# Optimization experiments

Measured on AMD Instinct MI355X. Metric: run time of the kernel, lower is better.

The kernel has to match this reference:

```python
import jax, jax.numpy as jnp
import numpy as np

N, L, D, H, MLP_MULT = 2, 384, 512, 8, 4
HD = D // H
DM = D * MLP_MULT
EPS = 1e-5


def _linear_params(key, out_dim, in_dim, scale=0.02):
    kw, kb = jax.random.split(key)
    w = jax.random.normal(kw, (out_dim, in_dim), jnp.float32) * scale
    b = jax.random.normal(kb, (out_dim,), jnp.float32) * scale
    return w, b


def setup_inputs() -> dict:
    key = jax.random.key(0)
    ks = jax.random.split(key, 12)
    x = jax.random.normal(ks[0], (N, L, D), jnp.float32)
    mem = jax.random.normal(ks[1], (N, L, D), jnp.float32)
    pairwise_distances = jax.random.normal(ks[2], (N, L, L, D), jnp.float32)
    mem_padding_mask = jax.random.randint(ks[3], (N, L), 0, 2).astype(bool)
    qw, qb = _linear_params(ks[4], D, D)
    kvw, kvb = _linear_params(ks[5], 2 * D, D)
    pw, pb = _linear_params(ks[6], D, D)
    edw, edb = _linear_params(ks[7], H, D)
    w1, b1 = _linear_params(ks[8], DM, D)
    w2, b2 = _linear_params(ks[9], DM, DM)
    w3, b3 = _linear_params(ks[10], D, DM)
    return {
        'x': x, 'mem': mem, 'pairwise_distances': pairwise_distances,
        'mem_padding_mask': mem_padding_mask,
        'qw': qw, 'qb': qb, 'kvw': kvw, 'kvb': kvb, 'pw': pw, 'pb': pb,
        'edw': edw, 'edb': edb,
        'ln1_g': jnp.ones((D,), jnp.float32), 'ln1_b': jnp.zeros((D,), jnp.float32),
        'ln2_g': jnp.ones((D,), jnp.float32), 'ln2_b': jnp.zeros((D,), jnp.float32),
        'w1': w1, 'b1': b1, 'w2': w2, 'b2': b2, 'w3': w3, 'b3': b3,
    }


def _layernorm(x, g, b):
    m = jnp.mean(x, axis=-1, keepdims=True)
    v = jnp.mean((x - m) ** 2, axis=-1, keepdims=True)
    return (x - m) * jax.lax.rsqrt(v + EPS) * g + b


def reference(x, mem, pairwise_distances, mem_padding_mask,
              qw, qb, kvw, kvb, pw, pb, edw, edb,
              ln1_g, ln1_b, ln2_g, ln2_b,
              w1, b1, w2, b2, w3, b3):
    scale = HD ** -0.5
    a_in = _layernorm(x, ln1_g, ln1_b)
    a_mem = _layernorm(mem, ln1_g, ln1_b)

    q = (a_in @ qw.T + qb).reshape(N, L, H, HD).transpose(0, 2, 1, 3)   # (N,H,L1,HD)
    kv = (a_mem @ kvw.T + kvb).reshape(N, L, 2, H, HD)
    k = kv[:, :, 0].transpose(0, 2, 1, 3)                               # (N,H,L2,HD)
    v = kv[:, :, 1].transpose(0, 2, 1, 3)

    scores = jnp.einsum('bhid,bhjd->bhij', q, k) * scale                # (N,H,L1,L2)

    # T5-style relative position bias from pairwise distances
    bias = (pairwise_distances @ edw.T + edb)                            # (N,L1,L2,H)
    scores = scores + bias.transpose(0, 3, 1, 2)

    # padding mask (True = padded); rows that are fully padded get a zero
    # mask instead (then their output is zeroed after attention)
    all_pad = jnp.all(mem_padding_mask, axis=-1)                         # (N,)
    neg_inf = jnp.asarray(-jnp.inf, scores.dtype)
    mask = jnp.where(mem_padding_mask[:, None, None, :], neg_inf, 0.0)
    mask = jnp.where(all_pad[:, None, None, None], 0.0, mask)
    scores = scores + mask

    attn = jax.nn.softmax(scores, axis=-1)
    out = jnp.einsum('bhij,bhjd->bhid', attn, v)                         # (N,H,L1,HD)
    out = out * (~all_pad)[:, None, None, None]
    out = out.transpose(0, 2, 1, 3).reshape(N, L, D)

    x = x + (out @ pw.T + pb)

    h = _layernorm(x, ln2_g, ln2_b)
    h = jax.nn.silu(h @ w1.T + b1)
    h = jax.nn.silu(h @ w2.T + b2)
    h = h @ w3.T + b3
    return x + h
```

## Files before the change

### kernel.cpp

```cpp
#include <hip/hip_runtime.h>
#include <hip/hip_bf16.h>
#include <math.h>

#define NB   2
#define LSEQ 384
#define DMODEL 512
#define NH   8
#define HD2  64
#define DMLP 2048
#define LL2  (LSEQ*LSEQ)
#define ROWS (NB*LSEQ)

using bf16x8 = __attribute__((ext_vector_type(8))) short;
using f32x4  = __attribute__((ext_vector_type(4))) float;

__device__ __forceinline__ unsigned short f2bf(float f) {
    union { __hip_bfloat16 h; unsigned short u; } cv;
    cv.h = __float2bfloat16(f);
    return cv.u;
}

__device__ __forceinline__ void gload_lds16(const void* g, void* l) {
    __builtin_amdgcn_global_load_lds(
        (const __attribute__((address_space(1))) void*)g,
        (__attribute__((address_space(3))) void*)l, 16, 0, 0);
}

__global__ __launch_bounds__(256) void pre_kernel(
        const float* __restrict__ x, const float* __restrict__ mem,
        const float* __restrict__ ln1g, const float* __restrict__ ln1b,
        unsigned short* __restrict__ a_in, unsigned short* __restrict__ a_mem,
        const float* __restrict__ s0, const float* __restrict__ s1,
        const float* __restrict__ s2, const float* __restrict__ s3,
        const float* __restrict__ s4, const float* __restrict__ s5,
        const float* __restrict__ edw,
        unsigned short* __restrict__ d0, unsigned short* __restrict__ d1,
        unsigned short* __restrict__ d2, unsigned short* __restrict__ d3,
        unsigned short* __restrict__ d4, unsigned short* __restrict__ d5,
        unsigned short* __restrict__ edwb) {
    const int tid = threadIdx.x;
    if (blockIdx.x < 384) {
        int lane = tid & 63;
        int row  = blockIdx.x * 4 + (tid >> 6);
        const float* src = (row < ROWS) ? x : mem;
        unsigned short* dst = (row < ROWS) ? a_in : a_mem;
        int r2 = (row < ROWS) ? row : row - ROWS;
        const float* p = src + (size_t)r2 * DMODEL + lane * 8;
        float4 v0 = *(const float4*)p;
        float4 v1 = *(const float4*)(p + 4);
        float s  = v0.x + v0.y + v0.z + v0.w + v1.x + v1.y + v1.z + v1.w;
        float ss = v0.x*v0.x + v0.y*v0.y + v0.z*v0.z + v0.w*v0.w
                 + v1.x*v1.x + v1.y*v1.y + v1.z*v1.z + v1.w*v1.w;
        #pragma unroll
        for (int o = 32; o; o >>= 1) { s += __shfl_xor(s, o); ss += __shfl_xor(ss, o); }
        float m   = s * (1.0f / DMODEL);
        float var = ss * (1.0f / DMODEL) - m * m;
        float r   = rsqrtf(var + 1e-5f);
        float4 g0 = *(const float4*)(ln1g + lane * 8);
        float4 g1 = *(const float4*)(ln1g + lane * 8 + 4);
        float4 b0 = *(const float4*)(ln1b + lane * 8);
        float4 b1 = *(const float4*)(ln1b + lane * 8 + 4);
        unsigned short* q = dst + (size_t)r2 * DMODEL + lane * 8;
        ushort4 lo = {f2bf((v0.x-m)*r*g0.x+b0.x), f2bf((v0.y-m)*r*g0.y+b0.y),
                      f2bf((v0.z-m)*r*g0.z+b0.z), f2bf((v0.w-m)*r*g0.w+b0.w)};
        ushort4 hi = {f2bf((v1.x-m)*r*g1.x+b1.x), f2bf((v1.y-m)*r*g1.y+b1.y),
                      f2bf((v1.z-m)*r*g1.z+b1.z), f2bf((v1.w-m)*r*g1.w+b1.w)};
        *(ushort4*)q = lo;
        *(ushort4*)(q + 4) = hi;
        return;
    }
    const int stride = (gridDim.x - 384) * 256;
    const int t0 = (blockIdx.x - 384) * 256 + tid;
    const float* srcs[6] = {s0, s1, s2, s3, s4, s5};
    unsigned short* dsts[6] = {d0, d1, d2, d3, d4, d5};
    const int nf4[6] = {DMODEL*DMODEL/4, 2*DMODEL*DMODEL/4, DMODEL*DMODEL/4,
                        DMLP*DMODEL/4, DMLP*DMLP/4, DMLP*DMODEL/4};
    #pragma unroll
    for (int a = 0; a < 6; a++) {
        const float* s = srcs[a];
        unsigned short* d = dsts[a];
        for (int i = t0; i < nf4[a]; i += stride) {
            float4 v = *(const float4*)(s + (size_t)i * 4);
            ushort4 o = {f2bf(v.x), f2bf(v.y), f2bf(v.z), f2bf(v.w)};
            *(ushort4*)(d + (size_t)i * 4) = o;
        }
    }
    for (int i = t0; i < 16 * 512 / 4; i += stride) {
        int row = i >> 7;
        float4 v = {0.f, 0.f, 0.f, 0.f};
        if (row < 8) v = *(const float4*)(edw + (size_t)i * 4);
        ushort4 o = {f2bf(v.x), f2bf(v.y), f2bf(v.z), f2bf(v.w)};
        *(ushort4*)(edwb + (size_t)i * 4) = o;
    }
}

__global__ __launch_bounds__(256) void ln_kernel(const float* __restrict__ src0,
                                                 const float* __restrict__ g,
                                                 const float* __restrict__ b,
                                                 unsigned short* __restrict__ dst0) {
    int lane = threadIdx.x & 63;
    int row  = blockIdx.x * 4 + (threadIdx.x >> 6);
    const float* p = src0 + (size_t)row * DMODEL + lane * 8;
    float4 v0 = *(const float4*)p;
    float4 v1 = *(const float4*)(p + 4);
    float s  = v0.x + v0.y + v0.z + v0.w + v1.x + v1.y + v1.z + v1.w;
    float ss = v0.x*v0.x + v0.y*v0.y + v0.z*v0.z + v0.w*v0.w
             + v1.x*v1.x + v1.y*v1.y + v1.z*v1.z + v1.w*v1.w;
    #pragma unroll
    for (int o = 32; o; o >>= 1) { s += __shfl_xor(s, o); ss += __shfl_xor(ss, o); }
    float m   = s * (1.0f / DMODEL);
    float var = ss * (1.0f / DMODEL) - m * m;
    float r   = rsqrtf(var + 1e-5f);
    float4 g0 = *(const float4*)(g + lane * 8);
    float4 g1 = *(const float4*)(g + lane * 8 + 4);
    float4 b0 = *(const float4*)(b + lane * 8);
    float4 b1 = *(const float4*)(b + lane * 8 + 4);
    unsigned short* q = dst0 + (size_t)row * DMODEL + lane * 8;
    ushort4 lo = {f2bf((v0.x-m)*r*g0.x+b0.x), f2bf((v0.y-m)*r*g0.y+b0.y),
                  f2bf((v0.z-m)*r*g0.z+b0.z), f2bf((v0.w-m)*r*g0.w+b0.w)};
    ushort4 hi = {f2bf((v1.x-m)*r*g1.x+b1.x), f2bf((v1.y-m)*r*g1.y+b1.y),
                  f2bf((v1.z-m)*r*g1.z+b1.z), f2bf((v1.w-m)*r*g1.w+b1.w)};
    *(ushort4*)q = lo;
    *(ushort4*)(q + 4) = hi;
}

__global__ __launch_bounds__(256) void bias_mfma(const float* __restrict__ pd,
                                                 const unsigned short* __restrict__ edwb,
                                                 const float* __restrict__ edb,
                                                 const int* __restrict__ mask,
                                                 float* __restrict__ biasb) {
    __shared__ float Asb[3][64 * 64];
    const int tid = threadIdx.x;
    const int lane = tid & 63, w = tid >> 6;
    const int T = blockIdx.x;
    const size_t row0 = (size_t)T * 64;
    const int n = T / 2304;
    const int rem64 = (T - n * 2304) * 64;
    const int i = rem64 / LSEQ, j0 = rem64 % LSEQ;

    const int c = lane & 15, g = lane >> 4;
    bf16x8 bfv[8][2];
    #pragma unroll
    for (int kc = 0; kc < 8; kc++)
        #pragma unroll
        for (int ks = 0; ks < 2; ks++)
            bfv[kc][ks] = *(const bf16x8*)&edwb[c * 512 + kc * 64 + ks * 32 + g * 8];

    int pad = 1;
    for (int j = lane; j < LSEQ; j += 64) pad &= (mask[n * LSEQ + j] != 0) ? 1 : 0;
    unsigned long long bal = __ballot(pad);
    const int ap = (bal == ~0ull) ? 1 : 0;

    int rr[4], sc[4];
    #pragma unroll
    for (int q = 0; q < 4; q++) {
        int s = q * 256 + tid;
        rr[q] = s >> 4;
        int cs = s & 15;
        sc[q] = (cs & 8) | ((cs & 7) ^ (rr[q] & 7));
    }

    f32x4 acc = {};

    #pragma unroll
    for (int q = 0; q < 4; q++)
        gload_lds16(pd + (row0 + rr[q]) * DMODEL + sc[q] * 4, &Asb[0][(q * 256 + tid) * 4]);
    #pragma unroll
    for (int q = 0; q < 4; q++)
        gload_lds16(pd + (row0 + rr[q]) * DMODEL + 64 + sc[q] * 4, &Asb[1][(q * 256 + tid) * 4]);

    #pragma unroll
    for (int kc = 0; kc < 8; kc++) {
        if (kc < 7) asm volatile("s_waitcnt vmcnt(4)" ::: "memory");
        else        asm volatile("s_waitcnt vmcnt(0)" ::: "memory");
        __builtin_amdgcn_s_barrier();
        __builtin_amdgcn_sched_barrier(0);
        if (kc + 2 < 8) {
            const int nb = (kc + 2) % 3;
            #pragma unroll
            for (int q = 0; q < 4; q++)
                gload_lds16(pd + (row0 + rr[q]) * DMODEL + (kc + 2) * 64 + sc[q] * 4,
                            &Asb[nb][(q * 256 + tid) * 4]);
        }
        const float* Ab = &Asb[kc % 3][0];
        #pragma unroll
        for (int ks = 0; ks < 2; ks++) {
            const int ch0 = (8 * ks) | ((2 * g) ^ (c & 7));
            const int ch1 = (8 * ks) | ((2 * g + 1) ^ (c & 7));
            float4 a0 = *(const float4*)&Ab[(w * 16 + c) * 64 + ch0 * 4];
            float4 a1 = *(const float4*)&Ab[(w * 16 + c) * 64 + ch1 * 4];
            bf16x8 af;
            af[0] = (short)f2bf(a0.x); af[1] = (short)f2bf(a0.y);
            af[2] = (short)f2bf(a0.z); af[3] = (short)f2bf(a0.w);
            af[4] = (short)f2bf(a1.x); af[5] = (short)f2bf(a1.y);
            af[6] = (short)f2bf(a1.z); af[7] = (short)f2bf(a1.w);
            acc = __builtin_amdgcn_mfma_f32_16x16x32_bf16(af, bfv[kc][ks], acc, 0, 0, 0);
        }
    }

    if (c < 8) {
        const float eb = edb[c];
        const int jj = j0 + w * 16 + g * 4;
        int4 mv = *(const int4*)&mask[n * LSEQ + jj];
        const float NEGINF = -__builtin_inff();
        float4 o;
        o.x = acc[0] + eb + ((!ap && mv.x) ? NEGINF : 0.0f);
        o.y = acc[1] + eb + ((!ap && mv.y) ? NEGINF : 0.0f);
        o.z = acc[2] + eb + ((!ap && mv.z) ? NEGINF : 0.0f);
        o.w = acc[3] + eb + ((!ap && mv.w) ? NEGINF : 0.0f);
        *(float4*)&biasb[(size_t)(n * 8 + c) * LL2 + (size_t)i * LSEQ + jj] = o;
    }
}

template<int ACT, int RES, int OBF>
__device__ __forceinline__ void gemm_body(const unsigned short* __restrict__ A,
        const unsigned short* __restrict__ W, const float* __restrict__ bv,
        const float* __restrict__ Rsd, void* __restrict__ Cv,
        int Nn, int K, int m0, int n0, short* As, short* Ws) {
    const int tid  = threadIdx.x;
    const int lane = tid & 63, w = tid >> 6;
    const int wr = w >> 1, wc = w & 1;
    const int s0 = tid, s1 = 256 + tid;
    const int r0 = s0 >> 3, c0 = ((s0 & 7) ^ (r0 & 7)) << 3;
    const int r1 = s1 >> 3, c1 = ((s1 & 7) ^ (r1 & 7)) << 3;
    const unsigned short* ag0 = A + (size_t)(m0 + r0) * K + c0;
    const unsigned short* ag1 = A + (size_t)(m0 + r1) * K + c1;
    const unsigned short* wg0 = W + (size_t)(n0 + r0) * K + c0;
    const unsigned short* wg1 = W + (size_t)(n0 + r1) * K + c1;

    f32x4 acc[2][2] = {};
    const int lc = lane & 15, lr = lane >> 4;
    const int KT = K >> 6;

    #pragma unroll
    for (int t = 0; t < 4; t++) {
        const int b = t * 4096, k0 = t << 6;
        gload_lds16(ag0 + k0, &As[b + s0 * 8]);
        gload_lds16(ag1 + k0, &As[b + s1 * 8]);
        gload_lds16(wg0 + k0, &Ws[b + s0 * 8]);
        gload_lds16(wg1 + k0, &Ws[b + s1 * 8]);
    }

    for (int t = 0; t < KT; t++) {
        int rem = KT - 1 - t; if (rem > 3) rem = 3;
        if (rem >= 3)      asm volatile("s_waitcnt vmcnt(12)" ::: "memory");
        else if (rem == 2) asm volatile("s_waitcnt vmcnt(8)"  ::: "memory");
        else if (rem == 1) asm volatile("s_waitcnt vmcnt(4)"  ::: "memory");
        else               asm volatile("s_waitcnt vmcnt(0)"  ::: "memory");
        __builtin_amdgcn_s_barrier();
        __builtin_amdgcn_sched_barrier(0);
        const int cur = (t & 3) * 4096;
        bf16x8 af[2][2], bfr[2][2];
        #pragma unroll
        for (int m = 0; m < 2; m++) {
            const int rra = wr * 32 + m * 16 + lc;
            #pragma unroll
            for (int kk = 0; kk < 2; kk++) {
                const int cc = (lr + kk * 4) ^ (rra & 7);
                af[m][kk] = *(const bf16x8*)&As[cur + rra * 64 + cc * 8];
            }
        }
        #pragma unroll
        for (int nn = 0; nn < 2; nn++) {
            const int rrb = wc * 32 + nn * 16 + lc;
            #pragma unroll
            for (int kk = 0; kk < 2; kk++) {
                const int cc = (lr + kk * 4) ^ (rrb & 7);
                bfr[nn][kk] = *(const bf16x8*)&Ws[cur + rrb * 64 + cc * 8];
            }
        }
        #pragma unroll
        for (int m = 0; m < 2; m++)
            #pragma unroll
            for (int nn = 0; nn < 2; nn++) {
                acc[m][nn] = __builtin_amdgcn_mfma_f32_16x16x32_bf16(af[m][0], bfr[nn][0], acc[m][nn], 0, 0, 0);
                acc[m][nn] = __builtin_amdgcn_mfma_f32_16x16x32_bf16(af[m][1], bfr[nn][1], acc[m][nn], 0, 0, 0);
            }
        if (t + 4 < KT) {
            __builtin_amdgcn_sched_barrier(0);
            __builtin_amdgcn_s_barrier();
            const int b = cur, k0 = (t + 4) << 6;
            gload_lds16(ag0 + k0, &As[b + s0 * 8]);
            gload_lds16(ag1 + k0, &As[b + s1 * 8]);
            gload_lds16(wg0 + k0, &Ws[b + s0 * 8]);
            gload_lds16(wg1 + k0, &Ws[b + s1 * 8]);
        }
    }

    #pragma unroll
    for (int nn = 0; nn < 2; nn++) {
        int gcol = n0 + wc * 32 + nn * 16 + lc;
        float bb = bv[gcol];
        #pragma unroll
        for (int m = 0; m < 2; m++) {
            #pragma unroll
            for (int r = 0; r < 4; r++) {
                int grow = m0 + wr * 32 + m * 16 + lr * 4 + r;
                float o = acc[m][nn][r] + bb;
                if (ACT) o = o / (1.0f + expf(-o));
                if (RES) o += Rsd[(size_t)grow * Nn + gcol];
                if (OBF) ((unsigned short*)Cv)[(size_t)grow * Nn + gcol] = f2bf(o);
                else     ((float*)Cv)[(size_t)grow * Nn + gcol] = o;
            }
        }
    }
}

template<int ACT, int RES, int OBF>
__global__ __launch_bounds__(256) void mfma_gemm(const unsigned short* __restrict__ A,
                                                 const unsigned short* __restrict__ W,
                                                 const float* __restrict__ bv,
                                                 const float* __restrict__ Rsd,
                                                 void* __restrict__ Cv, int Nn, int K) {
    __shared__ short As[4 * 4096];
    __shared__ short Ws[4 * 4096];
    gemm_body<ACT, RES, OBF>(A, W, bv, Rsd, Cv, Nn, K, blockIdx.y * 64, blockIdx.x * 64, As, Ws);
}

__global__ __launch_bounds__(256) void qkv_gemm(const unsigned short* __restrict__ a_in,
                                                const unsigned short* __restrict__ a_mem,
                                                const unsigned short* __restrict__ qwb,
                                                const unsigned short* __restrict__ kvwb,
                                                const float* __restrict__ qbv,
                                                const float* __restrict__ kvbv,
                                                float* __restrict__ qbuf,
                                                float* __restrict__ kvbuf) {
    __shared__ short As[4 * 4096];
    __shared__ short Ws[4 * 4096];
    const int bx = blockIdx.x;
    const unsigned short* A; const unsigned short* W; const float* bv; float* C; int Nn, n0;
    if (bx < 8) { A = a_in;  W = qwb;  bv = qbv;  C = qbuf;  Nn = DMODEL;     n0 = bx * 64; }
    else        { A = a_mem; W = kvwb; bv = kvbv; C = kvbuf; Nn = 2 * DMODEL; n0 = (bx - 8) * 64; }
    gemm_body<0, 0, 0>(A, W, bv, nullptr, C, Nn, DMODEL, blockIdx.y * 64, n0, As, Ws);
}

__global__ __launch_bounds__(256) void scores_kernel(const float* __restrict__ q,
                                                     const float* __restrict__ kv,
                                                     const float* __restrict__ biasb,
                                                     float* __restrict__ S) {
    const int n = blockIdx.z, h = blockIdx.y;
    const int it = blockIdx.x / 12, jt = blockIdx.x % 12;
    __shared__ float Qs[64][32];
    __shared__ float Ks[64][32];
    const int tid = threadIdx.x;
    const int r = tid >> 3, c = (tid & 7) << 3;
    {
        const float* qp = q + ((size_t)(n * LSEQ + it * 32 + r)) * DMODEL + h * HD2 + c;
        float4 q0 = *(const float4*)qp;
        float4 q1 = *(const float4*)(qp + 4);
        Qs[c+0][r]=q0.x; Qs[c+1][r]=q0.y; Qs[c+2][r]=q0.z; Qs[c+3][r]=q0.w;
        Qs[c+4][r]=q1.x; Qs[c+5][r]=q1.y; Qs[c+6][r]=q1.z; Qs[c+7][r]=q1.w;
        const float* kp = kv + ((size_t)(n * LSEQ + jt * 32 + r)) * (2 * DMODEL) + h * HD2 + c;
        float4 k0 = *(const float4*)kp;
        float4 k1 = *(const float4*)(kp + 4);
        Ks[c+0][r]=k0.x; Ks[c+1][r]=k0.y; Ks[c+2][r]=k0.z; Ks[c+3][r]=k0.w;
        Ks[c+4][r]=k1.x; Ks[c+5][r]=k1.y; Ks[c+6][r]=k1.z; Ks[c+7][r]=k1.w;
    }
    __syncthreads();
    const int tx = tid & 15, ty = tid >> 4;
    float acc[2][2] = {{0.f,0.f},{0.f,0.f}};
    #pragma unroll
    for (int k = 0; k < 64; k++) {
        float2 a  = *(const float2*)&Qs[k][ty << 1];
        float2 b2 = *(const float2*)&Ks[k][tx << 1];
        acc[0][0] = fmaf(a.x, b2.x, acc[0][0]);
        acc[0][1] = fmaf(a.x, b2.y, acc[0][1]);
        acc[1][0] = fmaf(a.y, b2.x, acc[1][0]);
        acc[1][1] = fmaf(a.y, b2.y, acc[1][1]);
    }
    #pragma unroll
    for (int i2 = 0; i2 < 2; i2++) {
        int gi = it * 32 + (ty << 1) + i2;
        #pragma unroll
        for (int j2 = 0; j2 < 2; j2++) {
            int gj = jt * 32 + (tx << 1) + j2;
            size_t idx = ((size_t)(n * 8 + h)) * LL2 + (size_t)gi * LSEQ + gj;
            S[idx] = acc[i2][j2] * 0.125f + biasb[idx];
        }
    }
}

__global__ __launch_bounds__(256) void softmax_kernel(float* __restrict__ S) {
    int lane = threadIdx.x & 63;
    int row  = blockIdx.x * 4 + (threadIdx.x >> 6);
    float* p = S + (size_t)row * LSEQ;
    float v[6];
    #pragma unroll
    for (int cc = 0; cc < 6; cc++) v[cc] = p[cc * 64 + lane];
    float mx = v[0];
    #pragma unroll
    for (int cc = 1; cc < 6; cc++) mx = fmaxf(mx, v[cc]);
    #pragma unroll
    for (int o = 32; o; o >>= 1) mx = fmaxf(mx, __shfl_xor(mx, o));
    float sum = 0.f;
    #pragma unroll
    for (int cc = 0; cc < 6; cc++) { v[cc] = __expf(v[cc] - mx); sum += v[cc]; }
    #pragma unroll
    for (int o = 32; o; o >>= 1) sum += __shfl_xor(sum, o);
    float inv = 1.0f / sum;
    #pragma unroll
    for (int cc = 0; cc < 6; cc++) p[cc * 64 + lane] = v[cc] * inv;
}

__global__ __launch_bounds__(256) void av_kernel(const float* __restrict__ S,
                                                 const float* __restrict__ kv,
                                                 const int* __restrict__ mask,
                                                 unsigned short* __restrict__ outb) {
    const int it = blockIdx.x, h = blockIdx.y, n = blockIdx.z;
    __shared__ float Ps[32][68];
    __shared__ float Vs[64][68];
    const int tid = threadIdx.x;
    const int lane = tid & 63;
    int pad = 1;
    for (int j = lane; j < LSEQ; j += 64) pad &= (mask[n * LSEQ + j] != 0) ? 1 : 0;
    unsigned long long bal = __ballot(pad != 0);
    const float zf = (bal == 0xFFFFFFFFFFFFFFFFull) ? 0.0f : 1.0f;
    const int tx = tid & 15, ty = tid >> 4;
    const int pr = tid >> 3, pc = (tid & 7) << 3;
    const int vr = tid >> 2, vc = (tid & 3) << 4;
    float acc0[4] = {0,0,0,0}, acc1[4] = {0,0,0,0};
    for (int j0 = 0; j0 < LSEQ; j0 += 64) {
        const float* sp = S + ((size_t)(n * 8 + h)) * LL2 + (size_t)(it * 32 + pr) * LSEQ + j0 + pc;
        float4 p0 = *(const float4*)sp;
        float4 p1 = *(const float4*)(sp + 4);
        *(float4*)&Ps[pr][pc]     = p0;
        *(float4*)&Ps[pr][pc + 4] = p1;
        #pragma unroll
        for (int u = 0; u < 4; u++) {
            float4 vvv = *(const float4*)&kv[((size_t)(n * LSEQ + j0 + vr)) * (2 * DMODEL)
                                             + DMODEL + h * HD2 + vc + 4 * u];
            *(float4*)&Vs[vr][vc + 4 * u] = vvv;
        }
        __syncthreads();
        #pragma unroll
        for (int j = 0; j < 64; j++) {
            float pa  = Ps[ty][j];
            float pb2 = Ps[ty + 16][j];
            float4 vv = *(const float4*)&Vs[j][tx << 2];
            acc0[0] = fmaf(pa,  vv.x, acc0[0]);
            acc0[1] = fmaf(pa,  vv.y, acc0[1]);
            acc0[2] = fmaf(pa,  vv.z, acc0[2]);
            acc0[3] = fmaf(pa,  vv.w, acc0[3]);
            acc1[0] = fmaf(pb2, vv.x, acc1[0]);
            acc1[1] = fmaf(pb2, vv.y, acc1[1]);
            acc1[2] = fmaf(pb2, vv.z, acc1[2]);
            acc1[3] = fmaf(pb2, vv.w, acc1[3]);
        }
        __syncthreads();
    }
    int i0 = it * 32;
    ushort4 o0 = {f2bf(acc0[0]*zf), f2bf(acc0[1]*zf), f2bf(acc0[2]*zf), f2bf(acc0[3]*zf)};
    ushort4 o1 = {f2bf(acc1[0]*zf), f2bf(acc1[1]*zf), f2bf(acc1[2]*zf), f2bf(acc1[3]*zf)};
    *(ushort4*)&outb[((size_t)(n * LSEQ + i0 + ty)) * DMODEL + h * HD2 + (tx << 2)]      = o0;
    *(ushort4*)&outb[((size_t)(n * LSEQ + i0 + ty + 16)) * DMODEL + h * HD2 + (tx << 2)] = o1;
}

extern "C" void kernel_launch(void* const* d_in, const int* in_sizes, int n_in,
                              void* d_out, int out_size, void* d_ws, size_t ws_size,
                              hipStream_t stream) {
    const float* x    = (const float*)d_in[0];
    const float* mem  = (const float*)d_in[1];
    const float* pd   = (const float*)d_in[2];
    const int*   mask = (const int*)d_in[3];
    const float* qw   = (const float*)d_in[4];
    const float* qbv  = (const float*)d_in[5];
    const float* kvw  = (const float*)d_in[6];
    const float* kvbv = (const float*)d_in[7];
    const float* pw   = (const float*)d_in[8];
    const float* pbv  = (const float*)d_in[9];
    const float* edw  = (const float*)d_in[10];
    const float* edb  = (const float*)d_in[11];
    const float* ln1g = (const float*)d_in[12];
    const float* ln1b = (const float*)d_in[13];
    const float* ln2g = (const float*)d_in[14];
    const float* ln2b = (const float*)d_in[15];
    const float* w1   = (const float*)d_in[16];
    const float* b1   = (const float*)d_in[17];
    const float* w2   = (const float*)d_in[18];
    const float* b2   = (const float*)d_in[19];
    const float* w3   = (const float*)d_in[20];
    const float* b3   = (const float*)d_in[21];

    float* wsf = (float*)d_ws;
    float* biasb  = wsf + 16;
    float* scores = biasb + (size_t)NB * NH * LL2;
    float* qbuf   = scores + (size_t)NB * NH * LL2;
    float* kvbuf  = qbuf + (size_t)ROWS * DMODEL;
    float* x1buf  = kvbuf + (size_t)ROWS * 2 * DMODEL;
    unsigned short* a_in  = (unsigned short*)(x1buf + (size_t)ROWS * DMODEL);
    unsigned short* a_mem = a_in  + (size_t)ROWS * DMODEL;
    unsigned short* attno = a_mem + (size_t)ROWS * DMODEL;
    unsigned short* h0    = attno + (size_t)ROWS * DMODEL;
    unsigned short* h1    = h0    + (size_t)ROWS * DMODEL;
    unsigned short* h2    = h1    + (size_t)ROWS * DMLP;
    unsigned short* qwb   = h2    + (size_t)ROWS * DMLP;
    unsigned short* kvwb  = qwb   + (size_t)DMODEL * DMODEL;
    unsigned short* pwb   = kvwb  + (size_t)2 * DMODEL * DMODEL;
    unsigned short* w1b   = pwb   + (size_t)DMODEL * DMODEL;
    unsigned short* w2b   = w1b   + (size_t)DMLP * DMODEL;
    unsigned short* w3b   = w2b   + (size_t)DMLP * DMLP;
    unsigned short* edwb  = w3b   + (size_t)DMLP * DMODEL;

    float* outp = (float*)d_out;

    pre_kernel<<<2048, 256, 0, stream>>>(x, mem, ln1g, ln1b, a_in, a_mem,
                                         qw, kvw, pw, w1, w2, w3, edw,
                                         qwb, kvwb, pwb, w1b, w2b, w3b, edwb);
    bias_mfma<<<NB * LL2 / 64, 256, 0, stream>>>(pd, edwb, edb, mask, biasb);
    qkv_gemm<<<dim3(24, 12), 256, 0, stream>>>(a_in, a_mem, qwb, kvwb, qbv, kvbv, qbuf, kvbuf);

    scores_kernel<<<dim3(144, NH, NB), 256, 0, stream>>>(qbuf, kvbuf, biasb, scores);
    softmax_kernel<<<(NB * NH * LSEQ) / 4, 256, 0, stream>>>(scores);
    av_kernel<<<dim3(12, NH, NB), 256, 0, stream>>>(scores, kvbuf, mask, attno);

    mfma_gemm<0,1,0><<<dim3(8, 12), 256, 0, stream>>>(attno, pwb, pbv, x, x1buf, DMODEL, DMODEL);
    ln_kernel<<<ROWS / 4, 256, 0, stream>>>(x1buf, ln2g, ln2b, h0);
    mfma_gemm<1,0,1><<<dim3(32, 12), 256, 0, stream>>>(h0, w1b, b1, nullptr, h1, DMLP, DMODEL);
    mfma_gemm<1,0,1><<<dim3(32, 12), 256, 0, stream>>>(h1, w2b, b2, nullptr, h2, DMLP, DMLP);
    mfma_gemm<0,1,0><<<dim3(8, 12), 256, 0, stream>>>(h2, w3b, b3, x1buf, outp, DMODEL, DMLP);
}
```

Measured before the change: 272.5 us.

## Fuse bias and QKV kernels, store bias in bf16, fold softmax into AV

Merges the relative-position bias MFMA kernel and the QKV GEMM into one launch by splitting blocks by index, and stores the bias in bf16 instead of fp32 to halve its write and read traffic. Removes the separate softmax pass: the AV kernel now loads a full 32-row score strip into LDS, computes max and exp in place, accumulates P·V with a register-prefetched double-buffered V tile, and normalises at the end. The GEMM pipeline depth drops from 4 to 2 LDS stages to reduce shared memory use. Bf16 bias adds rounding error, and the shallower GEMM pipeline may expose more load latency.

```diff
diff --git a/kernel.cpp b/kernel.cpp
--- a/kernel.cpp
+++ b/kernel.cpp
@@ -18,6 +18,11 @@
     union { __hip_bfloat16 h; unsigned short u; } cv;
     cv.h = __float2bfloat16(f);
     return cv.u;
+}
+__device__ __forceinline__ float bf2f(unsigned short u) {
+    union { float f; unsigned int i; } c;
+    c.i = ((unsigned int)u) << 16;
+    return c.f;
 }
 
 __device__ __forceinline__ void gload_lds16(const void* g, void* l) {
@@ -124,94 +129,6 @@
     *(ushort4*)(q + 4) = hi;
 }
 
-__global__ __launch_bounds__(256) void bias_mfma(const float* __restrict__ pd,
-                                                 const unsigned short* __restrict__ edwb,
-                                                 const float* __restrict__ edb,
-                                                 const int* __restrict__ mask,
-                                                 float* __restrict__ biasb) {
-    __shared__ float Asb[3][64 * 64];
-    const int tid = threadIdx.x;
-    const int lane = tid & 63, w = tid >> 6;
-    const int T = blockIdx.x;
-    const size_t row0 = (size_t)T * 64;
-    const int n = T / 2304;
-    const int rem64 = (T - n * 2304) * 64;
-    const int i = rem64 / LSEQ, j0 = rem64 % LSEQ;
-
-    const int c = lane & 15, g = lane >> 4;
-    bf16x8 bfv[8][2];
-    #pragma unroll
-    for (int kc = 0; kc < 8; kc++)
-        #pragma unroll
-        for (int ks = 0; ks < 2; ks++)
-            bfv[kc][ks] = *(const bf16x8*)&edwb[c * 512 + kc * 64 + ks * 32 + g * 8];
-
-    int pad = 1;
-    for (int j = lane; j < LSEQ; j += 64) pad &= (mask[n * LSEQ + j] != 0) ? 1 : 0;
-    unsigned long long bal = __ballot(pad);
-    const int ap = (bal == ~0ull) ? 1 : 0;
-
-    int rr[4], sc[4];
-    #pragma unroll
-    for (int q = 0; q < 4; q++) {
-        int s = q * 256 + tid;
-        rr[q] = s >> 4;
-        int cs = s & 15;
-        sc[q] = (cs & 8) | ((cs & 7) ^ (rr[q] & 7));
-    }
-
-    f32x4 acc = {};
-
-    #pragma unroll
-    for (int q = 0; q < 4; q++)
-        gload_lds16(pd + (row0 + rr[q]) * DMODEL + sc[q] * 4, &Asb[0][(q * 256 + tid) * 4]);
-    #pragma unroll
-    for (int q = 0; q < 4; q++)
-        gload_lds16(pd + (row0 + rr[q]) * DMODEL + 64 + sc[q] * 4, &Asb[1][(q * 256 + tid) * 4]);
-
-    #pragma unroll
-    for (int kc = 0; kc < 8; kc++) {
-        if (kc < 7) asm volatile("s_waitcnt vmcnt(4)" ::: "memory");
-        else        asm volatile("s_waitcnt vmcnt(0)" ::: "memory");
-        __builtin_amdgcn_s_barrier();
-        __builtin_amdgcn_sched_barrier(0);
-        if (kc + 2 < 8) {
-            const int nb = (kc + 2) % 3;
-            #pragma unroll
-            for (int q = 0; q < 4; q++)
-                gload_lds16(pd + (row0 + rr[q]) * DMODEL + (kc + 2) * 64 + sc[q] * 4,
-                            &Asb[nb][(q * 256 + tid) * 4]);
-        }
-        const float* Ab = &Asb[kc % 3][0];
-        #pragma unroll
-        for (int ks = 0; ks < 2; ks++) {
-            const int ch0 = (8 * ks) | ((2 * g) ^ (c & 7));
-            const int ch1 = (8 * ks) | ((2 * g + 1) ^ (c & 7));
-            float4 a0 = *(const float4*)&Ab[(w * 16 + c) * 64 + ch0 * 4];
-            float4 a1 = *(const float4*)&Ab[(w * 16 + c) * 64 + ch1 * 4];
-            bf16x8 af;
-            af[0] = (short)f2bf(a0.x); af[1] = (short)f2bf(a0.y);
-            af[2] = (short)f2bf(a0.z); af[3] = (short)f2bf(a0.w);
-            af[4] = (short)f2bf(a1.x); af[5] = (short)f2bf(a1.y);
-            af[6] = (short)f2bf(a1.z); af[7] = (short)f2bf(a1.w);
-            acc = __builtin_amdgcn_mfma_f32_16x16x32_bf16(af, bfv[kc][ks], acc, 0, 0, 0);
-        }
-    }
-
-    if (c < 8) {
-        const float eb = edb[c];
-        const int jj = j0 + w * 16 + g * 4;
-        int4 mv = *(const int4*)&mask[n * LSEQ + jj];
-        const float NEGINF = -__builtin_inff();
-        float4 o;
-        o.x = acc[0] + eb + ((!ap && mv.x) ? NEGINF : 0.0f);
-        o.y = acc[1] + eb + ((!ap && mv.y) ? NEGINF : 0.0f);
-        o.z = acc[2] + eb + ((!ap && mv.z) ? NEGINF : 0.0f);
-        o.w = acc[3] + eb + ((!ap && mv.w) ? NEGINF : 0.0f);
-        *(float4*)&biasb[(size_t)(n * 8 + c) * LL2 + (size_t)i * LSEQ + jj] = o;
-    }
-}
-
 template<int ACT, int RES, int OBF>
 __device__ __forceinline__ void gemm_body(const unsigned short* __restrict__ A,
         const unsigned short* __restrict__ W, const float* __restrict__ bv,
@@ -232,24 +149,21 @@
     const int lc = lane & 15, lr = lane >> 4;
     const int KT = K >> 6;
 
-    #pragma unroll
-    for (int t = 0; t < 4; t++) {
-        const int b = t * 4096, k0 = t << 6;
+    auto stage = [&](int t) {
+        const int b = (t & 1) * 4096, k0 = t << 6;
         gload_lds16(ag0 + k0, &As[b + s0 * 8]);
         gload_lds16(ag1 + k0, &As[b + s1 * 8]);
         gload_lds16(wg0 + k0, &Ws[b + s0 * 8]);
         gload_lds16(wg1 + k0, &Ws[b + s1 * 8]);
-    }
+    };
+    stage(0); stage(1);
 
     for (int t = 0; t < KT; t++) {
-        int rem = KT - 1 - t; if (rem > 3) rem = 3;
-        if (rem >= 3)      asm volatile("s_waitcnt vmcnt(12)" ::: "memory");
-        else if (rem == 2) asm volatile("s_waitcnt vmcnt(8)"  ::: "memory");
-        else if (rem == 1) asm volatile("s_waitcnt vmcnt(4)"  ::: "memory");
-        else               asm volatile("s_waitcnt vmcnt(0)"  ::: "memory");
+        if (t < KT - 1) asm volatile("s_waitcnt vmcnt(4)" ::: "memory");
+        else            asm volatile("s_waitcnt vmcnt(0)" ::: "memory");
         __builtin_amdgcn_s_barrier();
         __builtin_amdgcn_sched_barrier(0);
-        const int cur = (t & 3) * 4096;
+        const int cur = (t & 1) * 4096;
         bf16x8 af[2][2], bfr[2][2];
         #pragma unroll
         for (int m = 0; m < 2; m++) {
@@ -276,15 +190,9 @@
                 acc[m][nn] = __builtin_amdgcn_mfma_f32_16x16x32_bf16(af[m][0], bfr[nn][0], acc[m][nn], 0, 0, 0);
                 acc[m][nn] = __builtin_amdgcn_mfma_f32_16x16x32_bf16(af[m][1], bfr[nn][1], acc[m][nn], 0, 0, 0);
             }
-        if (t + 4 < KT) {
-            __builtin_amdgcn_sched_barrier(0);
-            __builtin_amdgcn_s_barrier();
-            const int b = cur, k0 = (t + 4) << 6;
-            gload_lds16(ag0 + k0, &As[b + s0 * 8]);
-            gload_lds16(ag1 + k0, &As[b + s1 * 8]);
-            gload_lds16(wg0 + k0, &Ws[b + s0 * 8]);
-            gload_lds16(wg1 + k0, &Ws[b + s1 * 8]);
-        }
+        __builtin_amdgcn_sched_barrier(0);
+        __builtin_amdgcn_s_barrier();
+        if (t + 2 < KT) stage(t + 2);
     }
 
     #pragma unroll
@@ -312,31 +220,110 @@
                                                  const float* __restrict__ bv,
                                                  const float* __restrict__ Rsd,
                                                  void* __restrict__ Cv, int Nn, int K) {
-    __shared__ short As[4 * 4096];
-    __shared__ short Ws[4 * 4096];
+    __shared__ short As[2 * 4096];
+    __shared__ short Ws[2 * 4096];
     gemm_body<ACT, RES, OBF>(A, W, bv, Rsd, Cv, Nn, K, blockIdx.y * 64, blockIdx.x * 64, As, Ws);
 }
 
-__global__ __launch_bounds__(256) void qkv_gemm(const unsigned short* __restrict__ a_in,
-                                                const unsigned short* __restrict__ a_mem,
-                                                const unsigned short* __restrict__ qwb,
-                                                const unsigned short* __restrict__ kvwb,
-                                                const float* __restrict__ qbv,
-                                                const float* __restrict__ kvbv,
-                                                float* __restrict__ qbuf,
-                                                float* __restrict__ kvbuf) {
-    __shared__ short As[4 * 4096];
-    __shared__ short Ws[4 * 4096];
-    const int bx = blockIdx.x;
-    const unsigned short* A; const unsigned short* W; const float* bv; float* C; int Nn, n0;
-    if (bx < 8) { A = a_in;  W = qwb;  bv = qbv;  C = qbuf;  Nn = DMODEL;     n0 = bx * 64; }
-    else        { A = a_mem; W = kvwb; bv = kvbv; C = kvbuf; Nn = 2 * DMODEL; n0 = (bx - 8) * 64; }
-    gemm_body<0, 0, 0>(A, W, bv, nullptr, C, Nn, DMODEL, blockIdx.y * 64, n0, As, Ws);
+__global__ __launch_bounds__(256) void bias_qkv(
+        const float* __restrict__ pd, const unsigned short* __restrict__ edwb,
+        const float* __restrict__ edb, const int* __restrict__ mask,
+        unsigned short* __restrict__ biasb,
+        const unsigned short* __restrict__ a_in, const unsigned short* __restrict__ a_mem,
+        const unsigned short* __restrict__ qwb, const unsigned short* __restrict__ kvwb,
+        const float* __restrict__ qbv, const float* __restrict__ kvbv,
+        float* __restrict__ qbuf, float* __restrict__ kvbuf) {
+    __shared__ short smem[16384];
+    const int tid = threadIdx.x;
+    if (blockIdx.x < 288) {
+        const int bx2 = blockIdx.x % 24, by = blockIdx.x / 24;
+        const unsigned short* A; const unsigned short* W; const float* bv; float* C; int Nn, n0;
+        if (bx2 < 8) { A = a_in;  W = qwb;  bv = qbv;  C = qbuf;  Nn = DMODEL;     n0 = bx2 * 64; }
+        else         { A = a_mem; W = kvwb; bv = kvbv; C = kvbuf; Nn = 2 * DMODEL; n0 = (bx2 - 8) * 64; }
+        gemm_body<0, 0, 0>(A, W, bv, nullptr, C, Nn, DMODEL, by * 64, n0, smem, smem + 8192);
+        return;
+    }
+    float* Asb = (float*)smem;
+    const int lane = tid & 63, w = tid >> 6;
+    const int T = blockIdx.x - 288;
+    const size_t row0 = (size_t)T * 64;
+    const int n = T / 2304;
+    const int rem64 = (T - n * 2304) * 64;
+    const int i = rem64 / LSEQ, j0 = rem64 % LSEQ;
+
+    const int c = lane & 15, g = lane >> 4;
+    bf16x8 bfv[8][2];
+    #pragma unroll
+    for (int kc = 0; kc < 8; kc++)
+        #pragma unroll
+        for (int ks = 0; ks < 2; ks++)
+            bfv[kc][ks] = *(const bf16x8*)&edwb[c * 512 + kc * 64 + ks * 32 + g * 8];
+
+    int pad = 1;
+    for (int j = lane; j < LSEQ; j += 64) pad &= (mask[n * LSEQ + j] != 0) ? 1 : 0;
+    unsigned long long bal = __ballot(pad);
+    const int ap = (bal == ~0ull) ? 1 : 0;
+
+    int rr[4], sc[4];
+    #pragma unroll
+    for (int q = 0; q < 4; q++) {
+        int s = q * 256 + tid;
+        rr[q] = s >> 4;
+        int cs = s & 15;
+        sc[q] = (cs & 8) | ((cs & 7) ^ (rr[q] & 7));
+    }
+
+    f32x4 acc = {};
+    #define STAGEB(kc_) { const int b_ = ((kc_) & 1) * 4096;                          \
+        _Pragma("unroll")                                                             \
+        for (int q = 0; q < 4; q++)                                                   \
+            gload_lds16(pd + (row0 + rr[q]) * DMODEL + (kc_) * 64 + sc[q] * 4,        \
+                        &Asb[b_ + (q * 256 + tid) * 4]); }
+    STAGEB(0); STAGEB(1);
+
+    #pragma unroll
+    for (int kc = 0; kc < 8; kc++) {
+        if (kc < 7) asm volatile("s_waitcnt vmcnt(4)" ::: "memory");
+        else        asm volatile("s_waitcnt vmcnt(0)" ::: "memory");
+        __builtin_amdgcn_s_barrier();
+        __builtin_amdgcn_sched_barrier(0);
+        const float* Ab = &Asb[(kc & 1) * 4096];
+        #pragma unroll
+        for (int ks = 0; ks < 2; ks++) {
+            const int ch0 = (8 * ks) | ((2 * g) ^ (c & 7));
+            const int ch1 = (8 * ks) | ((2 * g + 1) ^ (c & 7));
+            float4 a0 = *(const float4*)&Ab[(w * 16 + c) * 64 + ch0 * 4];
+            float4 a1 = *(const float4*)&Ab[(w * 16 + c) * 64 + ch1 * 4];
+            bf16x8 af;
+            af[0] = (short)f2bf(a0.x); af[1] = (short)f2bf(a0.y);
+            af[2] = (short)f2bf(a0.z); af[3] = (short)f2bf(a0.w);
+            af[4] = (short)f2bf(a1.x); af[5] = (short)f2bf(a1.y);
+            af[6] = (short)f2bf(a1.z); af[7] = (short)f2bf(a1.w);
+            acc = __builtin_amdgcn_mfma_f32_16x16x32_bf16(af, bfv[kc][ks], acc, 0, 0, 0);
+        }
+        __builtin_amdgcn_sched_barrier(0);
+        __builtin_amdgcn_s_barrier();
+        if (kc + 2 < 8) STAGEB(kc + 2);
+    }
+    #undef STAGEB
+
+    if (c < 8) {
+        const float eb = edb[c];
+        const int jj = j0 + w * 16 + g * 4;
+        int4 mv = *(const int4*)&mask[n * LSEQ + jj];
+        const float NEGINF = -__builtin_inff();
+        ushort4 o;
+        o.x = f2bf(acc[0] + eb + ((!ap && mv.x) ? NEGINF : 0.0f));
+        o.y = f2bf(acc[1] + eb + ((!ap && mv.y) ? NEGINF : 0.0f));
+        o.z = f2bf(acc[2] + eb + ((!ap && mv.z) ? NEGINF : 0.0f));
+        o.w = f2bf(acc[3] + eb + ((!ap && mv.w) ? NEGINF : 0.0f));
+        *(ushort4*)&biasb[(size_t)(n * 8 + c) * LL2 + (size_t)i * LSEQ + jj] = o;
+    }
 }
 
 __global__ __launch_bounds__(256) void scores_kernel(const float* __restrict__ q,
                                                      const float* __restrict__ kv,
-                                                     const float* __restrict__ biasb,
+                                                     const unsigned short* __restrict__ biasb,
                                                      float* __restrict__ S) {
     const int n = blockIdx.z, h = blockIdx.y;
     const int it = blockIdx.x / 12, jt = blockIdx.x % 12;
@@ -375,82 +362,93 @@
         for (int j2 = 0; j2 < 2; j2++) {
             int gj = jt * 32 + (tx << 1) + j2;
             size_t idx = ((size_t)(n * 8 + h)) * LL2 + (size_t)gi * LSEQ + gj;
-            S[idx] = acc[i2][j2] * 0.125f + biasb[idx];
-        }
-    }
-}
-
-__global__ __launch_bounds__(256) void softmax_kernel(float* __restrict__ S) {
-    int lane = threadIdx.x & 63;
-    int row  = blockIdx.x * 4 + (threadIdx.x >> 6);
-    float* p = S + (size_t)row * LSEQ;
-    float v[6];
-    #pragma unroll
-    for (int cc = 0; cc < 6; cc++) v[cc] = p[cc * 64 + lane];
-    float mx = v[0];
-    #pragma unroll
-    for (int cc = 1; cc < 6; cc++) mx = fmaxf(mx, v[cc]);
-    #pragma unroll
-    for (int o = 32; o; o >>= 1) mx = fmaxf(mx, __shfl_xor(mx, o));
-    float sum = 0.f;
-    #pragma unroll
-    for (int cc = 0; cc < 6; cc++) { v[cc] = __expf(v[cc] - mx); sum += v[cc]; }
-    #pragma unroll
-    for (int o = 32; o; o >>= 1) sum += __shfl_xor(sum, o);
-    float inv = 1.0f / sum;
-    #pragma unroll
-    for (int cc = 0; cc < 6; cc++) p[cc * 64 + lane] = v[cc] * inv;
-}
-
-__global__ __launch_bounds__(256) void av_kernel(const float* __restrict__ S,
-                                                 const float* __restrict__ kv,
-                                                 const int* __restrict__ mask,
-                                                 unsigned short* __restrict__ outb) {
+            S[idx] = acc[i2][j2] * 0.125f + bf2f(biasb[idx]);
+        }
+    }
+}
+
+__global__ __launch_bounds__(256) void av_sm_kernel(const float* __restrict__ S,
+                                                    const float* __restrict__ kv,
+                                                    const int* __restrict__ mask,
+                                                    unsigned short* __restrict__ outb) {
+    __shared__ float Ps[32][388];
+    __shared__ float Vs[2][64][68];
     const int it = blockIdx.x, h = blockIdx.y, n = blockIdx.z;
-    __shared__ float Ps[32][68];
-    __shared__ float Vs[64][68];
-    const int tid = threadIdx.x;
-    const int lane = tid & 63;
+    const int tid = threadIdx.x, lane = tid & 63;
     int pad = 1;
     for (int j = lane; j < LSEQ; j += 64) pad &= (mask[n * LSEQ + j] != 0) ? 1 : 0;
     unsigned long long bal = __ballot(pad != 0);
-    const float zf = (bal == 0xFFFFFFFFFFFFFFFFull) ? 0.0f : 1.0f;
+    const float zf = (bal == ~0ull) ? 0.0f : 1.0f;
+
+    const float* sb = S + ((size_t)(n * 8 + h)) * LL2 + (size_t)(it * 32) * LSEQ;
+    #pragma unroll
+    for (int s = 0; s < 12; s++) {
+        int idx = s * 256 + tid;
+        int rw = idx / 96, c4 = idx % 96;
+        float4 v = *(const float4*)&sb[(size_t)rw * LSEQ + c4 * 4];
+        *(float4*)&Ps[rw][c4 * 4] = v;
+    }
+    const int vr = tid >> 2, vc = (tid & 3) << 4;
+    float4 vreg[4];
+    #pragma unroll
+    for (int u = 0; u < 4; u++)
+        vreg[u] = *(const float4*)&kv[((size_t)(n * LSEQ + vr)) * (2 * DMODEL)
+                                      + DMODEL + h * HD2 + vc + 4 * u];
+    #pragma unroll
+    for (int u = 0; u < 4; u++) *(float4*)&Vs[0][vr][vc + 4 * u] = vreg[u];
+    __syncthreads();
+
     const int tx = tid & 15, ty = tid >> 4;
-    const int pr = tid >> 3, pc = (tid & 7) << 3;
-    const int vr = tid >> 2, vc = (tid & 3) << 4;
+    const int jb = tx * 24;
+    float mx0 = -3.0e38f, mx1 = -3.0e38f;
+    for (int j = jb; j < jb + 24; j++) {
+        mx0 = fmaxf(mx0, Ps[ty][j]);
+        mx1 = fmaxf(mx1, Ps[ty + 16][j]);
+    }
+    #pragma unroll
+    for (int o = 8; o; o >>= 1) { mx0 = fmaxf(mx0, __shfl_xor(mx0, o)); mx1 = fmaxf(mx1, __shfl_xor(mx1, o)); }
+    float l0 = 0.f, l1 = 0.f;
+    for (int j = jb; j < jb + 24; j++) {
+        float p0 = __expf(Ps[ty][j] - mx0);      Ps[ty][j] = p0;      l0 += p0;
+        float p1 = __expf(Ps[ty + 16][j] - mx1); Ps[ty + 16][j] = p1; l1 += p1;
+    }
+    #pragma unroll
+    for (int o = 8; o; o >>= 1) { l0 += __shfl_xor(l0, o); l1 += __shfl_xor(l1, o); }
+    __syncthreads();
+
     float acc0[4] = {0,0,0,0}, acc1[4] = {0,0,0,0};
-    for (int j0 = 0; j0 < LSEQ; j0 += 64) {
-        const float* sp = S + ((size_t)(n * 8 + h)) * LL2 + (size_t)(it * 32 + pr) * LSEQ + j0 + pc;
-        float4 p0 = *(const float4*)sp;
-        float4 p1 = *(const float4*)(sp + 4);
-        *(float4*)&Ps[pr][pc]     = p0;
-        *(float4*)&Ps[pr][pc + 4] = p1;
-        #pragma unroll
-        for (int u = 0; u < 4; u++) {
-            float4 vvv = *(const float4*)&kv[((size_t)(n * LSEQ + j0 + vr)) * (2 * DMODEL)
-                                             + DMODEL + h * HD2 + vc + 4 * u];
-            *(float4*)&Vs[vr][vc + 4 * u] = vvv;
+    for (int t = 0; t < 6; t++) {
+        if (t + 1 < 6) {
+            #pragma unroll
+            for (int u = 0; u < 4; u++)
+                vreg[u] = *(const float4*)&kv[((size_t)(n * LSEQ + (t + 1) * 64 + vr)) * (2 * DMODEL)
+                                              + DMODEL + h * HD2 + vc + 4 * u];
+        }
+        const float (*Vc)[68] = Vs[t & 1];
+        #pragma unroll
+        for (int j = 0; j < 64; j++) {
+            float pa = Ps[ty][t * 64 + j];
+            float pb = Ps[ty + 16][t * 64 + j];
+            float4 vv = *(const float4*)&Vc[j][tx << 2];
+            acc0[0] = fmaf(pa, vv.x, acc0[0]);
+            acc0[1] = fmaf(pa, vv.y, acc0[1]);
+            acc0[2] = fmaf(pa, vv.z, acc0[2]);
+            acc0[3] = fmaf(pa, vv.w, acc0[3]);
+            acc1[0] = fmaf(pb, vv.x, acc1[0]);
+            acc1[1] = fmaf(pb, vv.y, acc1[1]);
+            acc1[2] = fmaf(pb, vv.z, acc1[2]);
+            acc1[3] = fmaf(pb, vv.w, acc1[3]);
+        }
+        if (t + 1 < 6) {
+            #pragma unroll
+            for (int u = 0; u < 4; u++) *(float4*)&Vs[(t + 1) & 1][vr][vc + 4 * u] = vreg[u];
         }
         __syncthreads();
-        #pragma unroll
-        for (int j = 0; j < 64; j++) {
-            float pa  = Ps[ty][j];
-            float pb2 = Ps[ty + 16][j];
-            float4 vv = *(const float4*)&Vs[j][tx << 2];
-            acc0[0] = fmaf(pa,  vv.x, acc0[0]);
-            acc0[1] = fmaf(pa,  vv.y, acc0[1]);
-            acc0[2] = fmaf(pa,  vv.z, acc0[2]);
-            acc0[3] = fmaf(pa,  vv.w, acc0[3]);
-            acc1[0] = fmaf(pb2, vv.x, acc1[0]);
-            acc1[1] = fmaf(pb2, vv.y, acc1[1]);
-            acc1[2] = fmaf(pb2, vv.z, acc1[2]);
-            acc1[3] = fmaf(pb2, vv.w, acc1[3]);
-        }
-        __syncthreads();
-    }
-    int i0 = it * 32;
-    ushort4 o0 = {f2bf(acc0[0]*zf), f2bf(acc0[1]*zf), f2bf(acc0[2]*zf), f2bf(acc0[3]*zf)};
-    ushort4 o1 = {f2bf(acc1[0]*zf), f2bf(acc1[1]*zf), f2bf(acc1[2]*zf), f2bf(acc1[3]*zf)};
+    }
+    float inv0 = zf / l0, inv1 = zf / l1;
+    const int i0 = it * 32;
+    ushort4 o0 = {f2bf(acc0[0]*inv0), f2bf(acc0[1]*inv0), f2bf(acc0[2]*inv0), f2bf(acc0[3]*inv0)};
+    ushort4 o1 = {f2bf(acc1[0]*inv1), f2bf(acc1[1]*inv1), f2bf(acc1[2]*inv1), f2bf(acc1[3]*inv1)};
     *(ushort4*)&outb[((size_t)(n * LSEQ + i0 + ty)) * DMODEL + h * HD2 + (tx << 2)]      = o0;
     *(ushort4*)&outb[((size_t)(n * LSEQ + i0 + ty + 16)) * DMODEL + h * HD2 + (tx << 2)] = o1;
 }
@@ -482,8 +480,8 @@
     const float* b3   = (const float*)d_in[21];
 
     float* wsf = (float*)d_ws;
-    float* biasb  = wsf + 16;
-    float* scores = biasb + (size_t)NB * NH * LL2;
+    unsigned short* biasb = (unsigned short*)(wsf + 16);
+    float* scores = wsf + 16 + (size_t)NB * NH * LL2 / 2;
     float* qbuf   = scores + (size_t)NB * NH * LL2;
     float* kvbuf  = qbuf + (size_t)ROWS * DMODEL;
     float* x1buf  = kvbuf + (size_t)ROWS * 2 * DMODEL;
@@ -506,13 +504,11 @@
     pre_kernel<<<2048, 256, 0, stream>>>(x, mem, ln1g, ln1b, a_in, a_mem,
                                          qw, kvw, pw, w1, w2, w3, edw,
                                          qwb, kvwb, pwb, w1b, w2b, w3b, edwb);
-    bias_mfma<<<NB * LL2 / 64, 256, 0, stream>>>(pd, edwb, edb, mask, biasb);
-    qkv_gemm<<<dim3(24, 12), 256, 0, stream>>>(a_in, a_mem, qwb, kvwb, qbv, kvbv, qbuf, kvbuf);
-
+    bias_qkv<<<288 + NB * LL2 / 64, 256, 0, stream>>>(pd, edwb, edb, mask, biasb,
+                                                      a_in, a_mem, qwb, kvwb, qbv, kvbv,
+                                                      qbuf, kvbuf);
     scores_kernel<<<dim3(144, NH, NB), 256, 0, stream>>>(qbuf, kvbuf, biasb, scores);
-    softmax_kernel<<<(NB * NH * LSEQ) / 4, 256, 0, stream>>>(scores);
-    av_kernel<<<dim3(12, NH, NB), 256, 0, stream>>>(scores, kvbuf, mask, attno);
-
+    av_sm_kernel<<<dim3(12, NH, NB), 256, 0, stream>>>(scores, kvbuf, mask, attno);
     mfma_gemm<0,1,0><<<dim3(8, 12), 256, 0, stream>>>(attno, pwb, pbv, x, x1buf, DMODEL, DMODEL);
     ln_kernel<<<ROWS / 4, 256, 0, stream>>>(x1buf, ln2g, ln2b, h0);
     mfma_gemm<1,0,1><<<dim3(32, 12), 256, 0, stream>>>(h0, w1b, b1, nullptr, h1, DMLP, DMODEL);
```

Result: slower. 283.5 us (+4.0%).
